# Kernel tuning notes

Hardware: AMD Instinct MI355X
Metric: run time of the kernel (lower is better)

## Reference

```python
import jax, jax.numpy as jnp
import numpy as np
from jax import lax

S = 24  # number of depth slices / groups

def setup_inputs() -> dict:
    key = jax.random.key(0)
    k1, k2, k3 = jax.random.split(key, 3)
    x = jax.random.normal(k1, (8, 1, S, 256, 256), dtype=jnp.float32)
    # PyTorch ConvTranspose2d weight layout: [in_ch=1, out_ch=1, kH=4, kW=4], stacked over 24 slices
    w = jax.random.normal(k2, (S, 1, 1, 4, 4), dtype=jnp.float32) * 0.25  # ~ pytorch init scale
    b = jax.random.normal(k3, (S,), dtype=jnp.float32) * 0.25
    return {"x": x, "w": w, "b": b}

def _fwd(x, w, b):
    # x: [B, 1, S, H, W] -> treat the S slices as 24 groups of a single grouped
    # transposed conv (fuses the original loop of 24 tiny ConvTranspose2d ops).
    B, C, s, H, W = x.shape
    xs = x.reshape(B, s, H, W)  # [B, S, H, W], channel dim = S
    # transposed conv == dilated conv with spatially-flipped kernel,
    # padding = k - 1 - p = 4 - 1 - 1 = 2 on each side, lhs_dilation = stride = 2
    wf = w[:, 0, 0, ::-1, ::-1][:, None]  # [S, 1, 4, 4] OIHW, groups=S
    y = lax.conv_general_dilated(
        xs, wf,
        window_strides=(1, 1),
        padding=((2, 2), (2, 2)),
        lhs_dilation=(2, 2),
        dimension_numbers=("NCHW", "OIHW", "NCHW"),
        feature_group_count=s,
    )  # [B, S, 2H, 2W]
    y = y + b[None, :, None, None]
    return y[:, None]  # [B, 1, S, 2H, 2W]

def reference(x, w, b):
    return _fwd(x, w, b)
```

## Files before the change

### kernel.cpp

```cpp
#include <hip/hip_runtime.h>


#define NS 24
#define IH 256
#define IW 256
#define OHH 512
#define OWW 512

__global__ __launch_bounds__(256) void convt2x_shfl_kernel(
    const float* __restrict__ x, const float* __restrict__ w,
    const float* __restrict__ bias, float* __restrict__ out)
{
    const int b   = blockIdx.z;
    const int s   = blockIdx.y;
    const int lin = blockIdx.x * 256 + threadIdx.x;
    const int t   = lin & 63;
    const int r   = lin >> 6;

    const float* ximg = x + (size_t)(b * NS + s) * IH * IW;

    const float* wv = w + s * 16;
    float W[16];
    #pragma unroll
    for (int k = 0; k < 16; ++k) W[k] = wv[k];
    const float bb = bias[s];

    float X[3][6];
    #pragma unroll
    for (int i = 0; i < 3; ++i) {
        const int rr = r - 1 + i;
        float4 m = make_float4(0.f, 0.f, 0.f, 0.f);
        if (rr >= 0 && rr < IH)
            m = *(const float4*)(ximg + (size_t)rr * IW + 4 * t);
        const float lft = __shfl(m.w, t - 1);
        const float rgt = __shfl(m.x, t + 1);
        X[i][0] = (t == 0)  ? 0.f : lft;
        X[i][1] = m.x; X[i][2] = m.y; X[i][3] = m.z; X[i][4] = m.w;
        X[i][5] = (t == 63) ? 0.f : rgt;
    }

    float o0[8], o1[8];
    #pragma unroll
    for (int h = 0; h < 4; ++h) {
        o0[2*h]   = X[0][h]  *W[15] + X[0][h+1]*W[13]
                  + X[1][h]  *W[7]  + X[1][h+1]*W[5]  + bb;
        o0[2*h+1] = X[0][h+1]*W[14] + X[0][h+2]*W[12]
                  + X[1][h+1]*W[6]  + X[1][h+2]*W[4]  + bb;
        o1[2*h]   = X[1][h]  *W[11] + X[1][h+1]*W[9]
                  + X[2][h]  *W[3]  + X[2][h+1]*W[1]  + bb;
        o1[2*h+1] = X[1][h+1]*W[10] + X[1][h+2]*W[8]
                  + X[2][h+1]*W[2]  + X[2][h+2]*W[0]  + bb;
    }

    float* orow0 = out + ((size_t)(b * NS + s) * OHH + 2 * r)     * OWW + t * 8;
    float* orow1 = orow0 + OWW;
    ((float4*)orow0)[0] = make_float4(o0[0], o0[1], o0[2], o0[3]);
    ((float4*)orow0)[1] = make_float4(o0[4], o0[5], o0[6], o0[7]);
    ((float4*)orow1)[0] = make_float4(o1[0], o1[1], o1[2], o1[3]);
    ((float4*)orow1)[1] = make_float4(o1[4], o1[5], o1[6], o1[7]);
}

extern "C" void kernel_launch(void* const* d_in, const int* in_sizes, int n_in,
                              void* d_out, int out_size, void* d_ws, size_t ws_size,
                              hipStream_t stream) {
    const float* x    = (const float*)d_in[0];
    const float* w    = (const float*)d_in[1];
    const float* bias = (const float*)d_in[2];
    float* out        = (float*)d_out;

    dim3 grid(64, NS, 8);
    convt2x_shfl_kernel<<<grid, 256, 0, stream>>>(x, w, bias, out);
}
```

Baseline: 247.0 us.

## Coalesce stores via split half-row mapping, nontemporal writes, swizzled block order

```diff
diff --git a/kernel.cpp b/kernel.cpp
--- a/kernel.cpp
+++ b/kernel.cpp
@@ -7,13 +7,16 @@
 #define OHH 512
 #define OWW 512
 
-__global__ __launch_bounds__(256) void convt2x_shfl_kernel(
+typedef float f32x4 __attribute__((ext_vector_type(4)));
+
+__global__ __launch_bounds__(256) void convt2x_coal_kernel(
     const float* __restrict__ x, const float* __restrict__ w,
     const float* __restrict__ bias, float* __restrict__ out)
 {
-    const int b   = blockIdx.z;
-    const int s   = blockIdx.y;
-    const int lin = blockIdx.x * 256 + threadIdx.x;
+    const int b  = blockIdx.z;
+    const int s  = blockIdx.y;
+    const int xr  = ((blockIdx.x & 7) << 3) | (blockIdx.x >> 3);
+    const int lin = xr * 256 + threadIdx.x;
     const int t   = lin & 63;
     const int r   = lin >> 6;
 
@@ -25,39 +28,63 @@
     for (int k = 0; k < 16; ++k) W[k] = wv[k];
     const float bb = bias[s];
 
-    float X[3][6];
+    float X[3][2][4];
     #pragma unroll
     for (int i = 0; i < 3; ++i) {
         const int rr = r - 1 + i;
-        float4 m = make_float4(0.f, 0.f, 0.f, 0.f);
-        if (rr >= 0 && rr < IH)
-            m = *(const float4*)(ximg + (size_t)rr * IW + 4 * t);
-        const float lft = __shfl(m.w, t - 1);
-        const float rgt = __shfl(m.x, t + 1);
-        X[i][0] = (t == 0)  ? 0.f : lft;
-        X[i][1] = m.x; X[i][2] = m.y; X[i][3] = m.z; X[i][4] = m.w;
-        X[i][5] = (t == 63) ? 0.f : rgt;
+        float2 mA = make_float2(0.f, 0.f);
+        float2 mB = make_float2(0.f, 0.f);
+        if (rr >= 0 && rr < IH) {
+            const float* row = ximg + (size_t)rr * IW;
+            mA = *(const float2*)(row + 2 * t);
+            mB = *(const float2*)(row + 128 + 2 * t);
+        }
+        const float sAy = __shfl(mA.y, (t - 1) & 63);
+        const float sAx = __shfl(mA.x, (t + 1) & 63);
+        const float sBy = __shfl(mB.y, (t - 1) & 63);
+        const float sBx = __shfl(mB.x, (t + 1) & 63);
+        const float c127 = __shfl(mA.y, 63);
+        const float c128 = __shfl(mB.x, 0);
+
+        X[i][0][0] = (t == 0)  ? 0.f  : sAy;
+        X[i][0][1] = mA.x;
+        X[i][0][2] = mA.y;
+        X[i][0][3] = (t == 63) ? c128 : sAx;
+        X[i][1][0] = (t == 0)  ? c127 : sBy;
+        X[i][1][1] = mB.x;
+        X[i][1][2] = mB.y;
+        X[i][1][3] = (t == 63) ? 0.f  : sBx;
     }
 
-    float o0[8], o1[8];
+    float o0[2][4], o1[2][4];
     #pragma unroll
-    for (int h = 0; h < 4; ++h) {
-        o0[2*h]   = X[0][h]  *W[15] + X[0][h+1]*W[13]
-                  + X[1][h]  *W[7]  + X[1][h+1]*W[5]  + bb;
-        o0[2*h+1] = X[0][h+1]*W[14] + X[0][h+2]*W[12]
-                  + X[1][h+1]*W[6]  + X[1][h+2]*W[4]  + bb;
-        o1[2*h]   = X[1][h]  *W[11] + X[1][h+1]*W[9]
-                  + X[2][h]  *W[3]  + X[2][h+1]*W[1]  + bb;
-        o1[2*h+1] = X[1][h+1]*W[10] + X[1][h+2]*W[8]
-                  + X[2][h+1]*W[2]  + X[2][h+2]*W[0]  + bb;
+    for (int z = 0; z < 2; ++z) {
+        o0[z][0] = X[0][z][0]*W[15] + X[0][z][1]*W[13]
+                 + X[1][z][0]*W[7]  + X[1][z][1]*W[5]  + bb;
+        o0[z][1] = X[0][z][1]*W[14] + X[0][z][2]*W[12]
+                 + X[1][z][1]*W[6]  + X[1][z][2]*W[4]  + bb;
+        o0[z][2] = X[0][z][1]*W[15] + X[0][z][2]*W[13]
+                 + X[1][z][1]*W[7]  + X[1][z][2]*W[5]  + bb;
+        o0[z][3] = X[0][z][2]*W[14] + X[0][z][3]*W[12]
+                 + X[1][z][2]*W[6]  + X[1][z][3]*W[4]  + bb;
+        o1[z][0] = X[1][z][0]*W[11] + X[1][z][1]*W[9]
+                 + X[2][z][0]*W[3]  + X[2][z][1]*W[1]  + bb;
+        o1[z][1] = X[1][z][1]*W[10] + X[1][z][2]*W[8]
+                 + X[2][z][1]*W[2]  + X[2][z][2]*W[0]  + bb;
+        o1[z][2] = X[1][z][1]*W[11] + X[1][z][2]*W[9]
+                 + X[2][z][1]*W[3]  + X[2][z][2]*W[1]  + bb;
+        o1[z][3] = X[1][z][2]*W[10] + X[1][z][3]*W[8]
+                 + X[2][z][2]*W[2]  + X[2][z][3]*W[0]  + bb;
     }
 
-    float* orow0 = out + ((size_t)(b * NS + s) * OHH + 2 * r)     * OWW + t * 8;
-    float* orow1 = orow0 + OWW;
-    ((float4*)orow0)[0] = make_float4(o0[0], o0[1], o0[2], o0[3]);
-    ((float4*)orow0)[1] = make_float4(o0[4], o0[5], o0[6], o0[7]);
-    ((float4*)orow1)[0] = make_float4(o1[0], o1[1], o1[2], o1[3]);
-    ((float4*)orow1)[1] = make_float4(o1[4], o1[5], o1[6], o1[7]);
+    float* obase = out + ((size_t)(b * NS + s) * OHH + 2 * r) * OWW;
+    #pragma unroll
+    for (int z = 0; z < 2; ++z) {
+        f32x4 v0 = { o0[z][0], o0[z][1], o0[z][2], o0[z][3] };
+        f32x4 v1 = { o1[z][0], o1[z][1], o1[z][2], o1[z][3] };
+        __builtin_nontemporal_store(v0, (f32x4*)(obase + z * 256 + 4 * t));
+        __builtin_nontemporal_store(v1, (f32x4*)(obase + OWW + z * 256 + 4 * t));
+    }
 }
 
 extern "C" void kernel_launch(void* const* d_in, const int* in_sizes, int n_in,
@@ -69,5 +96,5 @@
     float* out        = (float*)d_out;
 
     dim3 grid(64, NS, 8);
-    convt2x_shfl_kernel<<<grid, 256, 0, stream>>>(x, w, bias, out);
+    convt2x_coal_kernel<<<grid, 256, 0, stream>>>(x, w, bias, out);
 }
```

After: 238.4 us. 3.5% less time.
